# Optimization experiments

Measured on AMD Instinct MI355X. Metric: run time of the kernel, lower is better.

## Reference

```python
import jax, jax.numpy as jnp
import numpy as np

NUM_TAGS = 512
START_TAG = 510
STOP_TAG = 511
NEG_INF = -10000.0
BATCH, SEQ_LEN = 64, 512


def setup_inputs() -> dict:
    key = jax.random.key(0)
    k1, k2, k3 = jax.random.split(key, 3)
    inputs = jax.random.normal(k1, (BATCH, SEQ_LEN, NUM_TAGS), dtype=jnp.float32)
    tags = jax.random.randint(k2, (BATCH, SEQ_LEN), 0, 510)
    transitions = jax.random.normal(k3, (NUM_TAGS, NUM_TAGS), dtype=jnp.float32)
    # faithful to __init__: start row and stop column clamped to -10000
    transitions = transitions.at[START_TAG, :].set(NEG_INF).at[:, STOP_TAG].set(NEG_INF)
    return {"inputs": inputs, "tags": tags, "transitions": transitions}


def _lse_source(x):
    # Faithful to the source's log_sum_exp: it subtracts the max but never
    # adds it back, i.e. returns logsumexp(x) - max(x) over the last dim.
    return jax.nn.logsumexp(x, axis=-1) - jnp.max(x, axis=-1)


def _log_denominator(inputs, transitions):
    B, L, T = inputs.shape
    fv0 = jnp.full((B, T), NEG_INF, dtype=inputs.dtype).at[:, START_TAG].set(0.0)

    def step(fv, emit_t):  # fv [B, T_prev], emit_t [B, T_next]
        # scores[b, next, prev] = fv[b, prev] + trans[next, prev] + emit[b, next]
        scores = fv[:, None, :] + transitions[None, :, :] + emit_t[:, :, None]
        return _lse_source(scores), None

    fv, _ = jax.lax.scan(step, fv0, jnp.transpose(inputs, (1, 0, 2)))
    terminal = fv + transitions[STOP_TAG][None, :]
    return _lse_source(terminal)  # [B]


def _log_numerator(inputs, tags, transitions):
    B, L, T = inputs.shape
    score = transitions[tags[:, 0], START_TAG]  # start -> first tag
    # transitions between consecutive tags: trans[tags[:, i+1], tags[:, i]]
    trans_scores = transitions[tags[:, 1:], tags[:, :-1]]  # [B, L-1]
    # emission: faithful to source, uses inputs at position i with tag at i+1
    emit_scores = jnp.take_along_axis(
        inputs[:, :-1, :], tags[:, 1:, None], axis=2
    )[..., 0]  # [B, L-1]
    score = score + jnp.sum(trans_scores + emit_scores, axis=1)
    score = score + transitions[STOP_TAG, tags[:, -1]]
    return score  # [B]


def reference(inputs, tags, transitions):
    log_den = _log_denominator(inputs, transitions)
    log_num = _log_numerator(inputs, tags, transitions)
    return jnp.sum(log_num - log_den)
```

## Files before the change

kernel.cpp:

```cpp
#include <hip/hip_runtime.h>
#include <math.h>
#include <stdint.h>

#define NTAGS 512
#define SEQL  512
#define BATCH 64
#define START_TAG 510
#define STOP_TAG  511
#define NEG_INF  -10000.0f

#define NB   64
#define BT   512
#define ROWS 8
#define REPS 8

#define WS_NUM_OFF  0
#define WS_SLOT_OFF 256
#define WS_BYTES    (WS_SLOT_OFF + 2 * REPS * NTAGS * 8)

#define AGLD(p) __hip_atomic_load((p), __ATOMIC_RELAXED, __HIP_MEMORY_SCOPE_AGENT)

__global__ __launch_bounds__(BT) void crf_fused(
    const float* __restrict__ inputs, const int* __restrict__ tags,
    const float* __restrict__ trans, void* __restrict__ ws,
    float* __restrict__ out)
{
    __shared__ float fv_lds[2][NTAGS];

    const int tid   = threadIdx.x;
    const int bid   = blockIdx.x;
    const int lane  = tid & 63;
    const int wave  = tid >> 6;
    const int myrow = bid * ROWS + wave;
    const int rep   = bid & (REPS - 1);

    float*    numacc = (float*)((char*)ws + WS_NUM_OFF);
    uint64_t* slots  = (uint64_t*)((char*)ws + WS_SLOT_OFF);

    float treg[8];
    {
        const float* trow = trans + (size_t)myrow * NTAGS;
        #pragma unroll
        for (int q = 0; q < 8; ++q) treg[q] = trow[lane + 64 * q];
    }

    float ns;
    {
        const int*   tg  = tags + bid * SEQL;
        const float* inb = inputs + (size_t)bid * SEQL * NTAGS;
        if (tid > 0) {
            const int cur = tg[tid], prev = tg[tid - 1];
            ns = trans[cur * NTAGS + prev] + inb[(size_t)(tid - 1) * NTAGS + cur];
        } else {
            ns = trans[tg[0] * NTAGS + START_TAG] + trans[STOP_TAG * NTAGS + tg[SEQL - 1]];
        }
    }
    #pragma unroll
    for (int off = 32; off; off >>= 1) ns += __shfl_xor(ns, off);
    if (lane == 0) atomicAdd(numacc, ns);
    __builtin_amdgcn_s_waitcnt(0);

    fv_lds[0][tid] = (tid == START_TAG) ? 0.0f : NEG_INF;
    __syncthreads();

    float mprev = (myrow == START_TAG) ? NEG_INF : 0.0f;

    for (int s = 0; s < SEQL; ++s) {
        const int pp = (s + 1) & 1;
        uint64_t* pubbase = slots + (size_t)pp * REPS * NTAGS;
        uint64_t* myslot  = slots + ((size_t)pp * REPS + rep) * NTAGS + tid;
        const unsigned want = (unsigned)(s + 1);
        const float* fvc = fv_lds[s & 1];

        uint64_t p = AGLD(myslot);

        float v[8];
        #pragma unroll
        for (int q = 0; q < 8; ++q)
            v[q] = fvc[lane + 64 * q] + treg[q];

        float m = fmaxf(fmaxf(fmaxf(v[0], v[1]), fmaxf(v[2], v[3])),
                        fmaxf(fmaxf(v[4], v[5]), fmaxf(v[6], v[7])));
        float ss = ((__expf(v[0] - mprev) + __expf(v[1] - mprev))
                  + (__expf(v[2] - mprev) + __expf(v[3] - mprev)))
                 + ((__expf(v[4] - mprev) + __expf(v[5] - mprev))
                  + (__expf(v[6] - mprev) + __expf(v[7] - mprev)));

        #pragma unroll
        for (int off = 32; off; off >>= 1) {
            const float ms  = __shfl_xor(m, off);
            const float sss = __shfl_xor(ss, off);
            m  = fmaxf(m, ms);
            ss += sss;
        }

        {
            const float nv = __logf(ss) + mprev - m;
            const uint64_t pk = ((uint64_t)want << 32) | (uint64_t)__float_as_uint(nv);
            if (lane < REPS)
                __hip_atomic_store(pubbase + (size_t)lane * NTAGS + myrow, pk,
                                   __ATOMIC_RELAXED, __HIP_MEMORY_SCOPE_AGENT);
        }
        mprev = m;

        if ((unsigned)(p >> 32) != want) {
            uint64_t q0 = AGLD(myslot), q1 = AGLD(myslot),
                     q2 = AGLD(myslot), q3 = AGLD(myslot);
            for (;;) {
                if ((unsigned)(q0 >> 32) == want) { p = q0; break; }
                q0 = AGLD(myslot);
                if ((unsigned)(q1 >> 32) == want) { p = q1; break; }
                q1 = AGLD(myslot);
                if ((unsigned)(q2 >> 32) == want) { p = q2; break; }
                q2 = AGLD(myslot);
                if ((unsigned)(q3 >> 32) == want) { p = q3; break; }
                q3 = AGLD(myslot);
            }
        }
        fv_lds[pp][tid] = __uint_as_float((unsigned)(p & 0xFFFFFFFFu));
        __syncthreads();
    }

    if (myrow == STOP_TAG) {
        const float* fvf = fv_lds[0];
        float v[8];
        #pragma unroll
        for (int q = 0; q < 8; ++q)
            v[q] = fvf[lane + 64 * q] + treg[q];
        float m = fmaxf(fmaxf(fmaxf(v[0], v[1]), fmaxf(v[2], v[3])),
                        fmaxf(fmaxf(v[4], v[5]), fmaxf(v[6], v[7])));
        float ss = ((__expf(v[0]) + __expf(v[1])) + (__expf(v[2]) + __expf(v[3])))
                 + ((__expf(v[4]) + __expf(v[5])) + (__expf(v[6]) + __expf(v[7])));
        #pragma unroll
        for (int off = 32; off; off >>= 1) {
            const float ms  = __shfl_xor(m, off);
            const float sss = __shfl_xor(ss, off);
            m  = fmaxf(m, ms);
            ss += sss;
        }
        if (lane == 0) {
            const float ld  = __logf(ss) - m;
            const float num = AGLD(numacc);
            out[0] = num - (float)BATCH * ld;
        }
    }
}

extern "C" void kernel_launch(void* const* d_in, const int* in_sizes, int n_in,
                              void* d_out, int out_size, void* d_ws, size_t ws_size,
                              hipStream_t stream)
{
    const float* inputs = (const float*)d_in[0];
    const int*   tags   = (const int*)  d_in[1];
    const float* trans  = (const float*)d_in[2];
    float* out = (float*)d_out;

    hipMemsetAsync(d_ws, 0, WS_BYTES, stream);

    crf_fused<<<NB, BT, 0, stream>>>(inputs, tags, trans, d_ws, out);
}
```

Baseline: 833.4 us.

## Co-locate all cooperating blocks on one XCD and exchange state via L2-local sc0 stores

Launches many surplus blocks, and each one reads its XCD id and takes a ticket. The first XCD to collect 64 blocks wins, and only those blocks run the recurrence. The others exit. With every participant on one XCD, the per-step forward-vector exchange can use sc0 global loads and stores that stay in the shared L2, replacing the replicated device-scope slots. A device-scope fallback copy is polled every 16 iterations. This removes cross-XCD coherence latency from each of the 512 serial steps. The costs are extra launched blocks and a dependence on hardware scheduling and the XCC_ID register; the scheme deadlocks if 64 blocks cannot be co-resident on one XCD.

Measured after the change: 3.250 ms. 3.9x slower.

```diff
diff --git a/kernel.cpp b/kernel.cpp
--- a/kernel.cpp
+++ b/kernel.cpp
@@ -9,33 +9,67 @@
 #define STOP_TAG  511
 #define NEG_INF  -10000.0f
 
-#define NB   64
+#define NBLK 1024
+#define P    64
 #define BT   512
 #define ROWS 8
-#define REPS 8
 
-#define WS_NUM_OFF  0
-#define WS_SLOT_OFF 256
-#define WS_BYTES    (WS_SLOT_OFF + 2 * REPS * NTAGS * 8)
+#define WS_NUM_OFF   0
+#define WS_CNT_OFF   16
+#define WS_WIN_OFF   48
+#define WS_FAST_OFF  256
+#define WS_LLC_OFF   (WS_FAST_OFF + 2 * NTAGS * 8)
+#define WS_BYTES     (WS_LLC_OFF + 2 * NTAGS * 8)
 
-#define AGLD(p) __hip_atomic_load((p), __ATOMIC_RELAXED, __HIP_MEMORY_SCOPE_AGENT)
+#define AGLD(p)   __hip_atomic_load((p), __ATOMIC_RELAXED, __HIP_MEMORY_SCOPE_AGENT)
+#define AGST(p,v) __hip_atomic_store((p), (v), __ATOMIC_RELAXED, __HIP_MEMORY_SCOPE_AGENT)
 
-__global__ __launch_bounds__(BT) void crf_fused(
+__device__ __forceinline__ uint64_t sc0_load(const uint64_t* p) {
+    uint64_t r;
+    asm volatile("global_load_dwordx2 %0, %1, off sc0\n\ts_waitcnt vmcnt(0)"
+                 : "=v"(r) : "v"(p) : "memory");
+    return r;
+}
+__device__ __forceinline__ void sc0_store(uint64_t* p, uint64_t v) {
+    asm volatile("global_store_dwordx2 %0, %1, off sc0" :: "v"(p), "v"(v) : "memory");
+}
+
+__global__ __launch_bounds__(BT, 8) void crf_fused(
     const float* __restrict__ inputs, const int* __restrict__ tags,
     const float* __restrict__ trans, void* __restrict__ ws,
     float* __restrict__ out)
 {
     __shared__ float fv_lds[2][NTAGS];
+    __shared__ int   s_tkt, s_win;
 
-    const int tid   = threadIdx.x;
-    const int bid   = blockIdx.x;
-    const int lane  = tid & 63;
-    const int wave  = tid >> 6;
-    const int myrow = bid * ROWS + wave;
-    const int rep   = bid & (REPS - 1);
+    const int tid  = threadIdx.x;
+    const int lane = tid & 63;
+    const int wave = tid >> 6;
 
     float*    numacc = (float*)((char*)ws + WS_NUM_OFF);
-    uint64_t* slots  = (uint64_t*)((char*)ws + WS_SLOT_OFF);
+    int*      cnt    = (int*)  ((char*)ws + WS_CNT_OFF);
+    int*      winner = (int*)  ((char*)ws + WS_WIN_OFF);
+    uint64_t* fast   = (uint64_t*)((char*)ws + WS_FAST_OFF);
+    uint64_t* llc    = (uint64_t*)((char*)ws + WS_LLC_OFF);
+
+    unsigned xcd;
+    asm volatile("s_getreg_b32 %0, hwreg(HW_REG_XCC_ID)" : "=s"(xcd));
+    xcd &= 7;
+    if (tid == 0) {
+        const int tkt = atomicAdd(&cnt[xcd], 1);
+        if (tkt == P - 1) atomicCAS(winner, 0, (int)xcd + 1);
+        s_tkt = tkt;
+    }
+    __syncthreads();
+    if (tid == 0) {
+        int w;
+        while ((w = AGLD(winner)) == 0) __builtin_amdgcn_s_sleep(8);
+        s_win = w;
+    }
+    __syncthreads();
+    const int role = s_tkt;
+    if ((int)xcd != s_win - 1 || role >= P) return;
+    const int myrow = role * ROWS + wave;
 
     float treg[8];
     {
@@ -46,8 +80,8 @@
 
     float ns;
     {
-        const int*   tg  = tags + bid * SEQL;
-        const float* inb = inputs + (size_t)bid * SEQL * NTAGS;
+        const int*   tg  = tags + role * SEQL;
+        const float* inb = inputs + (size_t)role * SEQL * NTAGS;
         if (tid > 0) {
             const int cur = tg[tid], prev = tg[tid - 1];
             ns = trans[cur * NTAGS + prev] + inb[(size_t)(tid - 1) * NTAGS + cur];
@@ -67,12 +101,12 @@
 
     for (int s = 0; s < SEQL; ++s) {
         const int pp = (s + 1) & 1;
-        uint64_t* pubbase = slots + (size_t)pp * REPS * NTAGS;
-        uint64_t* myslot  = slots + ((size_t)pp * REPS + rep) * NTAGS + tid;
+        uint64_t* fbuf = fast + (size_t)pp * NTAGS;
+        uint64_t* lbuf = llc  + (size_t)pp * NTAGS;
         const unsigned want = (unsigned)(s + 1);
         const float* fvc = fv_lds[s & 1];
 
-        uint64_t p = AGLD(myslot);
+        uint64_t p = sc0_load(&fbuf[tid]);
 
         float v[8];
         #pragma unroll
@@ -97,28 +131,27 @@
         {
             const float nv = __logf(ss) + mprev - m;
             const uint64_t pk = ((uint64_t)want << 32) | (uint64_t)__float_as_uint(nv);
-            if (lane < REPS)
-                __hip_atomic_store(pubbase + (size_t)lane * NTAGS + myrow, pk,
-                                   __ATOMIC_RELAXED, __HIP_MEMORY_SCOPE_AGENT);
+            if (lane == 0) {
+                sc0_store(&fbuf[myrow], pk);
+                AGST(&lbuf[myrow], pk);
+            }
         }
         mprev = m;
 
         if ((unsigned)(p >> 32) != want) {
-            uint64_t q0 = AGLD(myslot), q1 = AGLD(myslot),
-                     q2 = AGLD(myslot), q3 = AGLD(myslot);
+            int it = 0;
             for (;;) {
-                if ((unsigned)(q0 >> 32) == want) { p = q0; break; }
-                q0 = AGLD(myslot);
-                if ((unsigned)(q1 >> 32) == want) { p = q1; break; }
-                q1 = AGLD(myslot);
-                if ((unsigned)(q2 >> 32) == want) { p = q2; break; }
-                q2 = AGLD(myslot);
-                if ((unsigned)(q3 >> 32) == want) { p = q3; break; }
-                q3 = AGLD(myslot);
+                p = sc0_load(&fbuf[tid]);
+                if ((unsigned)(p >> 32) == want) break;
+                if (((++it) & 15) == 0) {
+                    const uint64_t p2 = AGLD(&lbuf[tid]);
+                    if ((unsigned)(p2 >> 32) == want) { p = p2; break; }
+                }
             }
         }
         fv_lds[pp][tid] = __uint_as_float((unsigned)(p & 0xFFFFFFFFu));
-        __syncthreads();
+
+        asm volatile("s_waitcnt lgkmcnt(0)\n\ts_barrier" ::: "memory");
     }
 
     if (myrow == STOP_TAG) {
@@ -157,5 +190,5 @@
 
     hipMemsetAsync(d_ws, 0, WS_BYTES, stream);
 
-    crf_fused<<<NB, BT, 0, stream>>>(inputs, tags, trans, d_ws, out);
+    crf_fused<<<NBLK, BT, 0, stream>>>(inputs, tags, trans, d_ws, out);
 }
```
